# Performance work log

Measured on AMD Instinct MI355X. Metric: run time of the kernel, lower is better.

## Reference

```python
import jax, jax.numpy as jnp
import numpy as np
import math

HID = 1152
NH = 16
HD = HID // NH            # 72
P = 2
DEPTH = 4
MLP_M = int(2.0 / 3.0 * int(HID * 4.0))  # 3072 (SwiGLU inner)
FREQ = 256
NCLS = 1000
ROPE_THETA = 10000.0


def rms_norm(x, w, eps=1e-6):
    return x * jax.lax.rsqrt(jnp.mean(jnp.square(x), axis=-1, keepdims=True) + eps) * w


def rotate_half(x):
    # interleaved pairs (a, b) -> (-b, a)
    x2 = x.reshape(x.shape[:-1] + (x.shape[-1] // 2, 2))
    a, b = x2[..., 0], x2[..., 1]
    return jnp.stack((-b, a), axis=-1).reshape(x.shape)


def make_rope(S, head_dim, theta=ROPE_THETA):
    # VisionRotaryEmbedder: per-axis rope dim = head_dim//2, 2 spatial axes concat
    d = head_dim // 2
    f = 1.0 / theta ** (jnp.arange(0, d, 2)[: d // 2].astype(jnp.float32) / d)
    fr = jnp.arange(S, dtype=jnp.float32)[:, None] * f[None, :]   # [S, d//2]
    fr = jnp.repeat(fr, 2, axis=-1)                               # [S, d]
    grid = jnp.concatenate(
        [jnp.broadcast_to(fr[:, None, :], (S, S, d)),
         jnp.broadcast_to(fr[None, :, :], (S, S, d))], axis=-1)   # [S, S, head_dim]
    grid = grid.reshape(S * S, head_dim)
    return jnp.cos(grid), jnp.sin(grid)


def timestep_embedding(t, dim=FREQ, max_period=10000.0):
    half = dim // 2
    freqs = jnp.exp(-math.log(max_period) * jnp.arange(half, dtype=jnp.float32) / half)
    args = t[:, None].astype(jnp.float32) * freqs[None, :]
    return jnp.concatenate([jnp.cos(args), jnp.sin(args)], axis=-1)


def setup_inputs() -> dict:
    key = jax.random.key(0)
    ks = jax.random.split(key, 24)
    s = 0.02
    B, C, H, W = 2, 4, 64, 64
    d = {
        'x': jax.random.normal(ks[0], (B, C, H, W), jnp.float32),
        't': jax.random.uniform(ks[1], (B,), jnp.float32),
        'y': jax.random.randint(ks[2], (B,), 0, NCLS),
        'patch_w': jax.random.normal(ks[3], (P * P * C, HID), jnp.float32) * s,
        'patch_b': jnp.zeros((HID,), jnp.float32),
        't_w1': jax.random.normal(ks[4], (FREQ, HID), jnp.float32) * s,
        't_b1': jnp.zeros((HID,), jnp.float32),
        't_w2': jax.random.normal(ks[5], (HID, HID), jnp.float32) * s,
        't_b2': jnp.zeros((HID,), jnp.float32),
        'y_table': jax.random.normal(ks[6], (NCLS + 1, HID), jnp.float32) * s,
        'norm1_w': jnp.ones((DEPTH, HID), jnp.float32),
        'qkv_w': jax.random.normal(ks[7], (DEPTH, HID, 3 * HID), jnp.float32) * s,
        'qkv_b': jnp.zeros((DEPTH, 3 * HID), jnp.float32),
        'out_w': jax.random.normal(ks[8], (DEPTH, HID, HID), jnp.float32) * s,
        'out_b': jnp.zeros((DEPTH, HID), jnp.float32),
        'norm2_w': jnp.ones((DEPTH, HID), jnp.float32),
        'mlp_w12': jax.random.normal(ks[9], (DEPTH, HID, 2 * MLP_M), jnp.float32) * s,
        'mlp_b12': jnp.zeros((DEPTH, 2 * MLP_M), jnp.float32),
        'mlp_w3': jax.random.normal(ks[10], (DEPTH, MLP_M, HID), jnp.float32) * s,
        'mlp_b3': jnp.zeros((DEPTH, HID), jnp.float32),
        'adaln_w': jax.random.normal(ks[11], (DEPTH, HID, 4 * HID), jnp.float32) * s,
        'adaln_b': jnp.zeros((DEPTH, 4 * HID), jnp.float32),
        'fnorm_w': jnp.ones((HID,), jnp.float32),
        'fadaln_w': jax.random.normal(ks[12], (HID, 2 * HID), jnp.float32) * s,
        'fadaln_b': jnp.zeros((2 * HID,), jnp.float32),
        'flin_w': jax.random.normal(ks[13], (HID, P * P * C), jnp.float32) * s,
        'flin_b': jnp.zeros((P * P * C,), jnp.float32),
    }
    return d


def reference(x, t, y, patch_w, patch_b, t_w1, t_b1, t_w2, t_b2, y_table,
              norm1_w, qkv_w, qkv_b, out_w, out_b, norm2_w,
              mlp_w12, mlp_b12, mlp_w3, mlp_b3, adaln_w, adaln_b,
              fnorm_w, fadaln_w, fadaln_b, flin_w, flin_b):
    B, C, H, W = x.shape
    S = H // P
    L = S * S
    # patchify -> [B, L, P*P*C] -> linear embed
    tok = x.reshape(B, C, S, P, S, P).transpose(0, 2, 4, 3, 5, 1).reshape(B, L, P * P * C)
    h = tok @ patch_w + patch_b
    # conditioning: timestep MLP + class embedding
    temb = timestep_embedding(t)
    temb = jax.nn.silu(temb @ t_w1 + t_b1) @ t_w2 + t_b2
    c = temb + y_table[y]
    c_silu = jax.nn.silu(c)
    cos, sin = make_rope(S, HD)  # [L, HD]
    scale = 1.0 / math.sqrt(HD)

    def block(hx, p):
        n1w, qw, qb, ow, ob, n2w, w12, b12, w3, b3, aw, ab = p
        mod = c_silu @ aw + ab  # [B, 4*HID]
        s_msa, g_msa, s_mlp, g_mlp = jnp.split(mod, 4, axis=-1)
        hmod = rms_norm(hx, n1w) * (1.0 + s_msa[:, None, :])
        qkv = (hmod @ qw + qb).reshape(B, L, 3, NH, HD)
        qkv = jnp.swapaxes(qkv, 1, 3)  # [B, NH, 3, L, HD]
        q, k, v = qkv[:, :, 0], qkv[:, :, 1], qkv[:, :, 2]
        q = q * cos + rotate_half(q) * sin
        k = k * cos + rotate_half(k) * sin
        w = jax.nn.softmax(jnp.einsum('bhqd,bhkd->bhqk', q, k) * scale, axis=-1)
        o = jnp.einsum('bhqk,bhkd->bhqd', w, v)
        o = jnp.swapaxes(o, 1, 2).reshape(B, L, HID) @ ow + ob
        hx = hx + g_msa[:, None, :] * o
        hmod2 = rms_norm(hx, n2w) * (1.0 + s_mlp[:, None, :])
        x12 = hmod2 @ w12 + b12
        x1, x2 = jnp.split(x12, 2, axis=-1)
        m = (jax.nn.silu(x1) * x2) @ w3 + b3
        hx = hx + g_mlp[:, None, :] * m
        return hx, None

    h, _ = jax.lax.scan(block, h, (norm1_w, qkv_w, qkv_b, out_w, out_b, norm2_w,
                                   mlp_w12, mlp_b12, mlp_w3, mlp_b3, adaln_w, adaln_b))

    # final layer: shift+scale modulation then zero-init linear (random here)
    fmod = c_silu @ fadaln_w + fadaln_b
    shift, fscale = jnp.split(fmod, 2, axis=-1)
    hf = rms_norm(h, fnorm_w) * (1.0 + fscale[:, None, :]) + shift[:, None, :]
    out = hf @ flin_w + flin_b  # [B, L, P*P*C]
    out = out.reshape(B, S, S, P, P, C).transpose(0, 5, 1, 3, 2, 4).reshape(B, C, H, W)
    return out
```

## Files before the change

### kernel.cpp

```cpp
#include <hip/hip_runtime.h>
#include <hip/hip_bf16.h>

#define HIDN 1152
#define NHEAD 16
#define HDIM 72
#define LTOK 1024
#define MTOK 2048
#define MLPM 3072

typedef short bf16x8 __attribute__((ext_vector_type(8)));
typedef float f32x4 __attribute__((ext_vector_type(4)));

__device__ __forceinline__ void gload16(const void* g, void* l) {
    __builtin_amdgcn_global_load_lds(
        (const __attribute__((address_space(1))) void*)g,
        (__attribute__((address_space(3))) void*)l,
        16, 0, 0);
}

__global__ __launch_bounds__(256) void k_patch(const float* __restrict__ x,
        const float* __restrict__ pw, const float* __restrict__ pb,
        float* __restrict__ h) {
    int m = blockIdx.x;
    int b = m >> 10, l = m & 1023;
    int si = l >> 5, sj = l & 31;
    __shared__ float toks[16];
    int tid = threadIdx.x;
    if (tid < 16) {
        int pi = tid >> 3, pj = (tid >> 2) & 1, c = tid & 3;
        toks[tid] = x[((size_t)(b*4 + c)*64 + si*2 + pi)*64 + sj*2 + pj];
    }
    __syncthreads();
    for (int o = tid; o < HIDN; o += 256) {
        float acc = pb[o];
        #pragma unroll
        for (int kk = 0; kk < 16; ++kk) acc += toks[kk] * pw[kk*HIDN + o];
        h[(size_t)m*HIDN + o] = acc;
    }
}

__global__ __launch_bounds__(256) void k_temb1_v2(const float* __restrict__ t,
        const float* __restrict__ w1, const float* __restrict__ b1,
        float* __restrict__ temb1) {
    int jt = blockIdx.x, b = blockIdx.y;
    int tid = threadIdx.x;
    __shared__ float emb[256];
    __shared__ float red[128];
    float tv = t[b];
    if (tid < 128) { float f = __expf(-logf(10000.f) * (float)tid / 128.f);        emb[tid] = cosf(tv * f); }
    else           { float f = __expf(-logf(10000.f) * (float)(tid - 128) / 128.f); emb[tid] = sinf(tv * f); }
    __syncthreads();
    int o = jt*128 + (tid & 127), s = tid >> 7;
    float acc = 0.f;
    for (int k = s*128; k < s*128 + 128; ++k) acc += emb[k] * w1[(size_t)k*HIDN + o];
    if (s) red[tid & 127] = acc;
    __syncthreads();
    if (!s) {
        float v = acc + red[tid] + b1[o];
        temb1[b*HIDN + o] = v / (1.f + __expf(-v));
    }
}

__global__ __launch_bounds__(256) void k_csilu_s1(const float* __restrict__ temb1,
        const float* __restrict__ w2, float* __restrict__ csilup) {
    int jt = blockIdx.x, kz = blockIdx.y;
    int tid = threadIdx.x;
    __shared__ float t1s[2][288];
    __shared__ float red[2][128];
    for (int i = tid; i < 576; i += 256)
        t1s[i/288][i%288] = temb1[(i/288)*HIDN + kz*288 + (i%288)];
    __syncthreads();
    int o = jt*128 + (tid & 127), s = tid >> 7;
    float a0 = 0.f, a1 = 0.f;
    for (int i = s*144; i < s*144 + 144; ++i) {
        float wv = w2[(size_t)(kz*288 + i)*HIDN + o];
        a0 += t1s[0][i]*wv; a1 += t1s[1][i]*wv;
    }
    if (s) { red[0][tid & 127] = a0; red[1][tid & 127] = a1; }
    __syncthreads();
    if (!s) {
        csilup[(kz*2 + 0)*HIDN + o] = a0 + red[0][tid];
        csilup[(kz*2 + 1)*HIDN + o] = a1 + red[1][tid];
    }
}

__global__ __launch_bounds__(128) void k_csilu_s2(const float* __restrict__ csilup,
        const float* __restrict__ b2, const float* __restrict__ ytab,
        const int* __restrict__ y, float* __restrict__ csilu) {
    int o = blockIdx.x*128 + threadIdx.x;
    int b = blockIdx.y;
    float acc = b2[o] + ytab[(size_t)y[b]*HIDN + o];
    #pragma unroll
    for (int kz = 0; kz < 4; ++kz) acc += csilup[(kz*2 + b)*HIDN + o];
    csilu[b*HIDN + o] = acc / (1.f + __expf(-acc));
}

__global__ __launch_bounds__(256) void k_cond_s1(const float* __restrict__ csilu,
        const float* __restrict__ adaln_w, const float* __restrict__ fadaln_w,
        float* __restrict__ condp) {
    int ct = blockIdx.x, kz = blockIdx.y;
    int tid = threadIdx.x;
    int c0 = ct*128;
    const float* Wb; int rstride;
    if (c0 < 18432) { int d = c0/4608; Wb = adaln_w + (size_t)d*HIDN*4608 + (c0 % 4608); rstride = 4608; }
    else            { Wb = fadaln_w + (c0 - 18432); rstride = 2304; }
    __shared__ float cs[2][288];
    __shared__ float red[2][128];
    for (int i = tid; i < 576; i += 256)
        cs[i/288][i%288] = csilu[(i/288)*HIDN + kz*288 + (i%288)];
    __syncthreads();
    int o = tid & 127, s = tid >> 7;
    float a0 = 0.f, a1 = 0.f;
    for (int i = s*144; i < s*144 + 144; ++i) {
        float wv = Wb[(size_t)(kz*288 + i)*rstride + o];
        a0 += cs[0][i]*wv; a1 += cs[1][i]*wv;
    }
    if (s) { red[0][o] = a0; red[1][o] = a1; }
    __syncthreads();
    if (!s) {
        condp[((size_t)kz*2 + 0)*20736 + c0 + o] = a0 + red[0][o];
        condp[((size_t)kz*2 + 1)*20736 + c0 + o] = a1 + red[1][o];
    }
}

__global__ __launch_bounds__(256) void k_cond_s2(const float* __restrict__ condp,
        const float* __restrict__ adaln_b, const float* __restrict__ fadaln_b,
        float* __restrict__ modb, float* __restrict__ fmod) {
    int c = blockIdx.x*256 + threadIdx.x;
    int b = blockIdx.y;
    float acc = 0.f;
    #pragma unroll
    for (int kz = 0; kz < 4; ++kz) acc += condp[((size_t)kz*2 + b)*20736 + c];
    if (c < 18432) {
        int d = c/4608, j = c%4608;
        modb[((size_t)d*2 + b)*4608 + j] = acc + adaln_b[(size_t)d*4608 + j];
    } else {
        int j = c - 18432;
        fmod[(size_t)b*2304 + j] = acc + fadaln_b[j];
    }
}

__global__ __launch_bounds__(256) void k_rope(float* __restrict__ cosb, float* __restrict__ sinb) {
    int idx = blockIdx.x*256 + threadIdx.x;
    if (idx >= LTOK*HDIM) return;
    int l = idx / HDIM, dd = idx % HDIM;
    int i = l >> 5, j = l & 31;
    int pos = (dd < 36) ? i : j;
    int mm = ((dd < 36) ? dd : dd - 36) >> 1;
    float f = __expf(-logf(10000.f) * (float)mm / 18.f);
    float fr = (float)pos * f;
    cosb[idx] = cosf(fr);
    sinb[idx] = sinf(fr);
}

__global__ __launch_bounds__(256) void k_rms(const float* __restrict__ hx,
        const float* __restrict__ nw, const float* __restrict__ smod,
        __hip_bfloat16* __restrict__ outp) {
    int m = blockIdx.x; int b = m >> 10;
    int tid = threadIdx.x;
    const float* row = hx + (size_t)m*HIDN;
    float part = 0.f;
    for (int j = tid; j < HIDN; j += 256) { float v = row[j]; part += v*v; }
    for (int off = 32; off; off >>= 1) part += __shfl_xor(part, off);
    __shared__ float wsum[4];
    if ((tid & 63) == 0) wsum[tid >> 6] = part;
    __syncthreads();
    float rs = rsqrtf((wsum[0]+wsum[1]+wsum[2]+wsum[3]) * (1.f/HIDN) + 1e-6f);
    const float* sb = smod + (size_t)b*4608;
    __hip_bfloat16* orow = outp + (size_t)m*HIDN;
    for (int j = tid; j < HIDN; j += 256)
        orow[j] = __float2bfloat16(row[j] * rs * nw[j] * (1.f + sb[j]));
}

__global__ __launch_bounds__(256) void k_castT(const float* __restrict__ W,
        __hip_bfloat16* __restrict__ Wt, int K, int N) {
    __shared__ float tile[32][33];
    int n0 = blockIdx.x*32, k0 = blockIdx.y*32;
    int tx = threadIdx.x, ty = threadIdx.y;
    for (int i = ty; i < 32; i += 8)
        tile[i][tx] = W[(size_t)(k0+i)*N + n0 + tx];
    __syncthreads();
    for (int i = ty; i < 32; i += 8)
        Wt[(size_t)(n0+i)*K + k0 + tx] = __float2bfloat16(tile[tx][i]);
}

template<int EPI, typename OutT>
__global__ __launch_bounds__(256) void k_gemm_bf16(
        const __hip_bfloat16* __restrict__ A,
        const __hip_bfloat16* __restrict__ Wt,
        const float* __restrict__ bias,
        OutT* __restrict__ C, int M, int N, int K,
        const float* __restrict__ gate) {
    __shared__ __hip_bfloat16 Asm[128*64];
    __shared__ __hip_bfloat16 Bsm[128*64];
    int tid = threadIdx.x;
    int lane = tid & 63, w = tid >> 6;
    int wr = w >> 1, wc = w & 1;
    int m0 = blockIdx.y * 128, n0 = blockIdx.x * 128;
    f32x4 acc[4][4] = {};
    int lr = lane >> 3, ls = lane & 7;
    int swz = ls ^ (lr & 7);
    int x7 = lane & 7;
    const __hip_bfloat16* Ag = A  + (size_t)(m0 + lr)*K + swz*8;
    const __hip_bfloat16* Bg = Wt + (size_t)(n0 + lr)*K + swz*8;
    for (int k0 = 0; k0 < K; k0 += 64) {
        #pragma unroll
        for (int i = 0; i < 4; ++i) {
            int seg = w*4 + i;
            gload16(Ag + (size_t)(seg*8)*K + k0, (char*)Asm + seg*1024);
            gload16(Bg + (size_t)(seg*8)*K + k0, (char*)Bsm + seg*1024);
        }
        __syncthreads();
        #pragma unroll
        for (int kk = 0; kk < 2; ++kk) {
            bf16x8 af[4], bfr[4];
            #pragma unroll
            for (int m = 0; m < 4; ++m) {
                int row = wr*64 + m*16 + (lane&15);
                af[m] = *(const bf16x8*)(Asm + row*64 + (((kk*4 + (lane>>4)) ^ x7) * 8));
            }
            #pragma unroll
            for (int n = 0; n < 4; ++n) {
                int col = wc*64 + n*16 + (lane&15);
                bfr[n] = *(const bf16x8*)(Bsm + col*64 + (((kk*4 + (lane>>4)) ^ x7) * 8));
            }
            #pragma unroll
            for (int m = 0; m < 4; ++m)
                #pragma unroll
                for (int n = 0; n < 4; ++n)
                    acc[m][n] = __builtin_amdgcn_mfma_f32_16x16x32_bf16(af[m], bfr[n], acc[m][n], 0, 0, 0);
        }
        __syncthreads();
    }
    int r0 = (lane >> 4) * 4;
    int ccol = lane & 15;
    #pragma unroll
    for (int m = 0; m < 4; ++m) {
        #pragma unroll
        for (int rr = 0; rr < 4; ++rr) {
            int row = m0 + wr*64 + m*16 + r0 + rr;
            int bi = row >> 10;
            #pragma unroll
            for (int n = 0; n < 4; ++n) {
                int col = n0 + wc*64 + n*16 + ccol;
                float val = acc[m][n][rr] + bias[col];
                if (EPI == 0) {
                    C[(size_t)row*N + col] = (OutT)__float2bfloat16(val);
                } else {
                    ((float*)C)[(size_t)row*N + col] += gate[(size_t)bi*4608 + col] * val;
                }
            }
        }
    }
}

__global__ __launch_bounds__(256) void k_gemm64(
        const __hip_bfloat16* __restrict__ A,
        const __hip_bfloat16* __restrict__ Wt,
        const float* __restrict__ bias,
        float* __restrict__ C, int M, int N, int K,
        const float* __restrict__ gate) {
    __shared__ __hip_bfloat16 Asm[64*64];
    __shared__ __hip_bfloat16 Bsm[128*64];
    int tid = threadIdx.x;
    int lane = tid & 63, w = tid >> 6;
    int wr = w >> 1, wc = w & 1;
    int m0 = blockIdx.y * 64, n0 = blockIdx.x * 128;
    f32x4 acc[2][4] = {};
    int lr = lane >> 3, ls = lane & 7;
    int swz = ls ^ (lr & 7);
    int x7 = lane & 7;
    const __hip_bfloat16* Ag = A  + (size_t)(m0 + lr)*K + swz*8;
    const __hip_bfloat16* Bg = Wt + (size_t)(n0 + lr)*K + swz*8;
    for (int k0 = 0; k0 < K; k0 += 64) {
        #pragma unroll
        for (int i = 0; i < 2; ++i) {
            int seg = w*2 + i;
            gload16(Ag + (size_t)(seg*8)*K + k0, (char*)Asm + seg*1024);
        }
        #pragma unroll
        for (int i = 0; i < 4; ++i) {
            int seg = w*4 + i;
            gload16(Bg + (size_t)(seg*8)*K + k0, (char*)Bsm + seg*1024);
        }
        __syncthreads();
        #pragma unroll
        for (int kk = 0; kk < 2; ++kk) {
            bf16x8 af[2], bfr[4];
            #pragma unroll
            for (int m = 0; m < 2; ++m) {
                int row = wr*32 + m*16 + (lane&15);
                af[m] = *(const bf16x8*)(Asm + row*64 + (((kk*4 + (lane>>4)) ^ x7) * 8));
            }
            #pragma unroll
            for (int n = 0; n < 4; ++n) {
                int col = wc*64 + n*16 + (lane&15);
                bfr[n] = *(const bf16x8*)(Bsm + col*64 + (((kk*4 + (lane>>4)) ^ x7) * 8));
            }
            #pragma unroll
            for (int m = 0; m < 2; ++m)
                #pragma unroll
                for (int n = 0; n < 4; ++n)
                    acc[m][n] = __builtin_amdgcn_mfma_f32_16x16x32_bf16(af[m], bfr[n], acc[m][n], 0, 0, 0);
        }
        __syncthreads();
    }
    int r0 = (lane >> 4) * 4;
    int ccol = lane & 15;
    #pragma unroll
    for (int m = 0; m < 2; ++m) {
        #pragma unroll
        for (int rr = 0; rr < 4; ++rr) {
            int row = m0 + wr*32 + m*16 + r0 + rr;
            int bi = row >> 10;
            #pragma unroll
            for (int n = 0; n < 4; ++n) {
                int col = n0 + wc*64 + n*16 + ccol;
                float val = acc[m][n][rr] + bias[col];
                C[(size_t)row*N + col] += gate[(size_t)bi*4608 + col] * val;
            }
        }
    }
}

__global__ __launch_bounds__(256) void k_ropesplit(const __hip_bfloat16* __restrict__ qkv,
        const float* __restrict__ cosb, const float* __restrict__ sinb,
        __hip_bfloat16* __restrict__ q, __hip_bfloat16* __restrict__ k,
        __hip_bfloat16* __restrict__ v) {
    int idx = blockIdx.x*256 + threadIdx.x;
    if (idx >= 2*NHEAD*LTOK*36) return;
    int dp = idx % 36;
    int l  = (idx / 36) % LTOK;
    int h  = (idx / (36*LTOK)) % NHEAD;
    int b  = idx / (36*LTOK*NHEAD);
    int d0 = dp*2;
    size_t src = (size_t)(b*LTOK + l)*3456 + h*HDIM + d0;
    float qe = __bfloat162float(qkv[src]),        qo = __bfloat162float(qkv[src+1]);
    float ke = __bfloat162float(qkv[src+HIDN]),   ko = __bfloat162float(qkv[src+HIDN+1]);
    float ce = cosb[l*HDIM+d0], co = cosb[l*HDIM+d0+1];
    float se = sinb[l*HDIM+d0], so = sinb[l*HDIM+d0+1];
    size_t dst = (size_t)((b*NHEAD + h)*LTOK + l)*HDIM + d0;
    q[dst]   = __float2bfloat16(qe*ce - qo*se);
    q[dst+1] = __float2bfloat16(qo*co + qe*so);
    k[dst]   = __float2bfloat16(ke*ce - ko*se);
    k[dst+1] = __float2bfloat16(ko*co + ke*so);
    size_t vdst = ((size_t)(b*NHEAD + h)*HDIM + d0)*LTOK + l;
    v[vdst]        = qkv[src+2*HIDN];
    v[vdst+LTOK]   = qkv[src+2*HIDN+1];
}

__global__ __launch_bounds__(256) void k_attn_mfma(
        const __hip_bfloat16* __restrict__ q,
        const __hip_bfloat16* __restrict__ k,
        const __hip_bfloat16* __restrict__ vt,
        __hip_bfloat16* __restrict__ o) {
    int blk = blockIdx.x;
    int qt = blk & 15, h = (blk >> 4) & 15, b = blk >> 8;
    const float scale = 0.117851130f;
    __shared__ __hip_bfloat16 Ksm[2][64*72];
    __shared__ __hip_bfloat16 Vsm[2][72*64];
    __shared__ __hip_bfloat16 Psm[4][16*72];
    int tid = threadIdx.x, lane = tid & 63, w = tid >> 6;
    int l15 = lane & 15, g = lane >> 4;
    const __hip_bfloat16* qg = q  + ((size_t)(b*NHEAD + h)*LTOK + qt*64)*HDIM;
    const __hip_bfloat16* kg = k  + (size_t)(b*NHEAD + h)*LTOK*HDIM;
    const __hip_bfloat16* vg = vt + (size_t)(b*NHEAD + h)*HDIM*LTOK;
    const bf16x8 z = {};

    bf16x8 qf[3];
    {
        const __hip_bfloat16* qrow = qg + (w*16 + l15)*HDIM;
        qf[0] = *(const bf16x8*)(qrow + g*8);
        qf[1] = *(const bf16x8*)(qrow + 32 + g*8);
        qf[2] = (g == 0) ? *(const bf16x8*)(qrow + 64) : z;
    }
    int vsw  = ((lane & 7) ^ (lane >> 3)) * 8;
    int vrow = lane >> 3;

    f32x4 oacc[5] = {};
    float mold[4] = {-1e30f, -1e30f, -1e30f, -1e30f};
    float lsum[4] = {};

    {
        const __hip_bfloat16* ktg = kg;
        const __hip_bfloat16* vtg = vg;
        for (int s = w; s < 9; s += 4) {
            gload16(ktg + s*512 + lane*8, (char*)&Ksm[0][0] + s*1024);
            gload16(vtg + (size_t)(s*8 + vrow)*LTOK + vsw, (char*)&Vsm[0][0] + s*1024);
        }
    }
    __syncthreads();

    for (int kt2 = 0; kt2 < 16; ++kt2) {
        int cur = kt2 & 1;
        if (kt2 < 15) {
            const __hip_bfloat16* ktg = kg + (size_t)(kt2+1)*64*HDIM;
            const __hip_bfloat16* vtg = vg + (kt2+1)*64;
            for (int s = w; s < 9; s += 4) {
                gload16(ktg + s*512 + lane*8, (char*)&Ksm[cur^1][0] + s*1024);
                gload16(vtg + (size_t)(s*8 + vrow)*LTOK + vsw, (char*)&Vsm[cur^1][0] + s*1024);
            }
        }
        const __hip_bfloat16* Kc = Ksm[cur];
        const __hip_bfloat16* Vc = Vsm[cur];
        f32x4 st[4] = {};
        __builtin_amdgcn_s_setprio(1);
        #pragma unroll
        for (int t = 0; t < 4; ++t) {
            const __hip_bfloat16* krow = Kc + (t*16 + l15)*72;
            bf16x8 kf0 = *(const bf16x8*)(krow + g*8);
            bf16x8 kf1 = *(const bf16x8*)(krow + 32 + g*8);
            bf16x8 kf2 = (g == 0) ? *(const bf16x8*)(krow + 64) : z;
            st[t] = __builtin_amdgcn_mfma_f32_16x16x32_bf16(qf[0], kf0, st[t], 0, 0, 0);
            st[t] = __builtin_amdgcn_mfma_f32_16x16x32_bf16(qf[1], kf1, st[t], 0, 0, 0);
            st[t] = __builtin_amdgcn_mfma_f32_16x16x32_bf16(qf[2], kf2, st[t], 0, 0, 0);
        }
        __builtin_amdgcn_s_setprio(0);
        #pragma unroll
        for (int r = 0; r < 4; ++r) {
            float mt = fmaxf(fmaxf(st[0][r], st[1][r]), fmaxf(st[2][r], st[3][r]));
            mt = fmaxf(mt, __shfl_xor(mt, 1));
            mt = fmaxf(mt, __shfl_xor(mt, 2));
            mt = fmaxf(mt, __shfl_xor(mt, 4));
            mt = fmaxf(mt, __shfl_xor(mt, 8));
            float mn = fmaxf(mold[r], mt);
            float corr = __expf((mold[r] - mn) * scale);
            mold[r] = mn;
            lsum[r] *= corr;
            #pragma unroll
            for (int dt = 0; dt < 5; ++dt) oacc[dt][r] *= corr;
            float rs = 0.f;
            #pragma unroll
            for (int t = 0; t < 4; ++t) {
                float p = __expf((st[t][r] - mn) * scale);
                rs += p;
                Psm[w][(g*4 + r)*72 + t*16 + l15] = __float2bfloat16(p);
            }
            rs += __shfl_xor(rs, 1);
            rs += __shfl_xor(rs, 2);
            rs += __shfl_xor(rs, 4);
            rs += __shfl_xor(rs, 8);
            lsum[r] += rs;
        }
        bf16x8 pa0 = *(const bf16x8*)(&Psm[w][l15*72 + g*8]);
        bf16x8 pa1 = *(const bf16x8*)(&Psm[w][l15*72 + 32 + g*8]);
        int cswz = (l15 & 7)*8;
        __builtin_amdgcn_s_setprio(1);
        #pragma unroll
        for (int dt = 0; dt < 5; ++dt) {
            int row = dt*16 + l15;
            bool valid = (dt < 4) | (l15 < 8);
            bf16x8 vf0 = valid ? *(const bf16x8*)(Vc + row*64 + ((g*8) ^ cswz)) : z;
            bf16x8 vf1 = valid ? *(const bf16x8*)(Vc + row*64 + ((32 + g*8) ^ cswz)) : z;
            oacc[dt] = __builtin_amdgcn_mfma_f32_16x16x32_bf16(pa0, vf0, oacc[dt], 0, 0, 0);
            oacc[dt] = __builtin_amdgcn_mfma_f32_16x16x32_bf16(pa1, vf1, oacc[dt], 0, 0, 0);
        }
        __builtin_amdgcn_s_setprio(0);
        __syncthreads();
    }
    #pragma unroll
    for (int r = 0; r < 4; ++r) {
        float inv = 1.f / lsum[r];
        int row = qt*64 + w*16 + g*4 + r;
        __hip_bfloat16* op = o + ((size_t)b*LTOK + row)*HIDN + h*HDIM;
        #pragma unroll
        for (int dt = 0; dt < 5; ++dt) {
            int d = dt*16 + l15;
            if (d < HDIM) op[d] = __float2bfloat16(oacc[dt][r] * inv);
        }
    }
}

__global__ __launch_bounds__(256) void k_glu(const __hip_bfloat16* __restrict__ x12,
        __hip_bfloat16* __restrict__ mh) {
    int idx = blockIdx.x*256 + threadIdx.x;
    int m = idx / 384, jj = (idx % 384)*8;
    bf16x8 v1 = *(const bf16x8*)(x12 + (size_t)m*6144 + jj);
    bf16x8 v2 = *(const bf16x8*)(x12 + (size_t)m*6144 + MLPM + jj);
    bf16x8 ov;
    #pragma unroll
    for (int i = 0; i < 8; ++i) {
        short s1 = v1[i], s2 = v2[i];
        float x1 = __bfloat162float(*(__hip_bfloat16*)&s1);
        float x2 = __bfloat162float(*(__hip_bfloat16*)&s2);
        __hip_bfloat16 r = __float2bfloat16(x1 / (1.f + __expf(-x1)) * x2);
        ov[i] = *(short*)&r;
    }
    *(bf16x8*)(mh + (size_t)m*MLPM + jj) = ov;
}

__global__ __launch_bounds__(256) void k_final(const float* __restrict__ hx,
        const float* __restrict__ fnw, const float* __restrict__ fmod,
        const float* __restrict__ flw, const float* __restrict__ flb,
        float* __restrict__ out) {
    int m = blockIdx.x; int b = m >> 10, l = m & 1023;
    int tid = threadIdx.x;
    const float* row = hx + (size_t)m*HIDN;
    float part = 0.f;
    for (int j = tid; j < HIDN; j += 256) { float v2 = row[j]; part += v2*v2; }
    for (int off = 32; off; off >>= 1) part += __shfl_xor(part, off);
    __shared__ float wsum[4];
    __shared__ float hfs[HIDN];
    __shared__ float red[4][16];
    if ((tid & 63) == 0) wsum[tid >> 6] = part;
    __syncthreads();
    float rs = rsqrtf((wsum[0]+wsum[1]+wsum[2]+wsum[3]) * (1.f/HIDN) + 1e-6f);
    const float* fm = fmod + (size_t)b*2304;
    for (int j = tid; j < HIDN; j += 256)
        hfs[j] = row[j] * rs * fnw[j] * (1.f + fm[HIDN + j]) + fm[j];
    __syncthreads();
    float pacc[16] = {};
    for (int j = tid; j < HIDN; j += 256) {
        float hv = hfs[j];
        #pragma unroll
        for (int kk = 0; kk < 16; ++kk) pacc[kk] += hv * flw[j*16 + kk];
    }
    #pragma unroll
    for (int kk = 0; kk < 16; ++kk)
        for (int off = 32; off; off >>= 1) pacc[kk] += __shfl_xor(pacc[kk], off);
    if ((tid & 63) == 0) {
        int w = tid >> 6;
        #pragma unroll
        for (int kk = 0; kk < 16; ++kk) red[w][kk] = pacc[kk];
    }
    __syncthreads();
    if (tid < 16) {
        float val = red[0][tid] + red[1][tid] + red[2][tid] + red[3][tid] + flb[tid];
        int pi = tid >> 3, pj = (tid >> 2) & 1, c = tid & 3;
        int si = l >> 5, sj = l & 31;
        out[((size_t)(b*4 + c)*64 + si*2 + pi)*64 + sj*2 + pj] = val;
    }
}

extern "C" void kernel_launch(void* const* d_in, const int* in_sizes, int n_in,
                              void* d_out, int out_size, void* d_ws, size_t ws_size,
                              hipStream_t stream) {
    const float* x        = (const float*)d_in[0];
    const float* t        = (const float*)d_in[1];
    const int*   y        = (const int*)  d_in[2];
    const float* patch_w  = (const float*)d_in[3];
    const float* patch_b  = (const float*)d_in[4];
    const float* t_w1     = (const float*)d_in[5];
    const float* t_b1     = (const float*)d_in[6];
    const float* t_w2     = (const float*)d_in[7];
    const float* t_b2     = (const float*)d_in[8];
    const float* y_table  = (const float*)d_in[9];
    const float* norm1_w  = (const float*)d_in[10];
    const float* qkv_w    = (const float*)d_in[11];
    const float* qkv_b    = (const float*)d_in[12];
    const float* out_w    = (const float*)d_in[13];
    const float* out_b    = (const float*)d_in[14];
    const float* norm2_w  = (const float*)d_in[15];
    const float* mlp_w12  = (const float*)d_in[16];
    const float* mlp_b12  = (const float*)d_in[17];
    const float* mlp_w3   = (const float*)d_in[18];
    const float* mlp_b3   = (const float*)d_in[19];
    const float* adaln_w  = (const float*)d_in[20];
    const float* adaln_b  = (const float*)d_in[21];
    const float* fnorm_w  = (const float*)d_in[22];
    const float* fadaln_w = (const float*)d_in[23];
    const float* fadaln_b = (const float*)d_in[24];
    const float* flin_w   = (const float*)d_in[25];
    const float* flin_b   = (const float*)d_in[26];

    char* base = (char*)d_ws;
    float*          hx    = (float*)(base);
    __hip_bfloat16* qkvbf = (__hip_bfloat16*)(base +  9437184);
    __hip_bfloat16* qbf   = (__hip_bfloat16*)(base + 34603008);
    __hip_bfloat16* kbf   = (__hip_bfloat16*)(base + 39321600);
    __hip_bfloat16* vbf   = (__hip_bfloat16*)(base + 44040192);
    __hip_bfloat16* hbf   = (__hip_bfloat16*)(base + 48758784);
    __hip_bfloat16* mhbf  = qbf;
    __hip_bfloat16* wtb   = (__hip_bfloat16*)(base + 53477376);
    float* temb1 = (float*)(base + 85327872);
    float* csilu = (float*)(base + 85337088);
    float* modb  = (float*)(base + 85346304);
    float* fmod  = (float*)(base + 85493760);
    float* cosb  = (float*)(base + 85512192);
    float* sinb  = (float*)(base + 85807104);
    float* condp = (float*)(base + 86102016);
    float* csilup= (float*)(base + 86765568);

    __hip_bfloat16* wt_qkv = wtb;
    __hip_bfloat16* wt_out = wt_qkv + 3456*1152;
    __hip_bfloat16* wt_m12 = wt_out + 1152*1152;
    __hip_bfloat16* wt_m3  = wt_m12 + 6144*1152;

    k_patch<<<2048, 256, 0, stream>>>(x, patch_w, patch_b, hx);
    k_temb1_v2<<<dim3(9,2), 256, 0, stream>>>(t, t_w1, t_b1, temb1);
    k_csilu_s1<<<dim3(9,4), 256, 0, stream>>>(temb1, t_w2, csilup);
    k_csilu_s2<<<dim3(9,2), 128, 0, stream>>>(csilup, t_b2, y_table, y, csilu);
    k_cond_s1<<<dim3(162,4), 256, 0, stream>>>(csilu, adaln_w, fadaln_w, condp);
    k_cond_s2<<<dim3(81,2), 256, 0, stream>>>(condp, adaln_b, fadaln_b, modb, fmod);
    k_rope<<<288, 256, 0, stream>>>(cosb, sinb);

    for (int d = 0; d < 4; ++d) {
        const float* modd = modb + (size_t)d*2*4608;
        k_castT<<<dim3(108,36), dim3(32,8), 0, stream>>>(qkv_w  + (size_t)d*HIDN*3456, wt_qkv, HIDN, 3456);
        k_castT<<<dim3( 36,36), dim3(32,8), 0, stream>>>(out_w  + (size_t)d*HIDN*HIDN, wt_out, HIDN, HIDN);
        k_castT<<<dim3(192,36), dim3(32,8), 0, stream>>>(mlp_w12+ (size_t)d*HIDN*6144, wt_m12, HIDN, 6144);
        k_castT<<<dim3( 36,96), dim3(32,8), 0, stream>>>(mlp_w3 + (size_t)d*MLPM*HIDN, wt_m3,  MLPM, HIDN);

        k_rms<<<2048, 256, 0, stream>>>(hx, norm1_w + d*HIDN, modd + 0*HIDN, hbf);
        k_gemm_bf16<0, __hip_bfloat16><<<dim3(27,16), 256, 0, stream>>>(hbf, wt_qkv,
                qkv_b + d*3456, qkvbf, MTOK, 3456, HIDN, nullptr);
        k_ropesplit<<<4608, 256, 0, stream>>>(qkvbf, cosb, sinb, qbf, kbf, vbf);
        k_attn_mfma<<<512, 256, 0, stream>>>(qbf, kbf, vbf, hbf);
        k_gemm64<<<dim3(9,32), 256, 0, stream>>>(hbf, wt_out,
                out_b + d*HIDN, hx, MTOK, HIDN, HIDN, modd + 1*HIDN);
        k_rms<<<2048, 256, 0, stream>>>(hx, norm2_w + d*HIDN, modd + 2*HIDN, hbf);
        k_gemm_bf16<0, __hip_bfloat16><<<dim3(48,16), 256, 0, stream>>>(hbf, wt_m12,
                mlp_b12 + d*6144, qkvbf, MTOK, 6144, HIDN, nullptr);
        k_glu<<<3072, 256, 0, stream>>>(qkvbf, mhbf);
        k_gemm64<<<dim3(9,32), 256, 0, stream>>>(mhbf, wt_m3,
                mlp_b3 + d*HIDN, hx, MTOK, HIDN, MLPM, modd + 3*HIDN);
    }
    k_final<<<2048, 256, 0, stream>>>(hx, fnorm_w, fmod, flin_w, flin_b, (float*)d_out);
}
```

Measured before the change: 1.097 ms.

## Batch weight casts, fuse SwiGLU into GEMM epilogue, split-K attention with merge

Result: slower. 1.126 ms (+2.6%).

```diff
diff --git a/kernel.cpp b/kernel.cpp
--- a/kernel.cpp
+++ b/kernel.cpp
@@ -172,16 +172,29 @@
         orow[j] = __float2bfloat16(row[j] * rs * nw[j] * (1.f + sb[j]));
 }
 
-__global__ __launch_bounds__(256) void k_castT(const float* __restrict__ W,
-        __hip_bfloat16* __restrict__ Wt, int K, int N) {
+__global__ __launch_bounds__(256) void k_castT_all(
+        const float* __restrict__ qkv_w, const float* __restrict__ out_w,
+        const float* __restrict__ m12_w, const float* __restrict__ m3_w,
+        __hip_bfloat16* __restrict__ wtb) {
     __shared__ float tile[32][33];
-    int n0 = blockIdx.x*32, k0 = blockIdx.y*32;
+    int bid = blockIdx.x;
+    int layer = bid / 15552, r = bid % 15552;
+    const float* W; __hip_bfloat16* Wt; int K, N, nt, t; bool glu = false;
+    __hip_bfloat16* bl = wtb + (size_t)layer*15925248;
+    if (r < 3888)       { t = r;         nt = 108; K = 1152; N = 3456; W = qkv_w + (size_t)layer*K*N; Wt = bl; }
+    else if (r < 5184)  { t = r - 3888;  nt = 36;  K = 1152; N = 1152; W = out_w + (size_t)layer*K*N; Wt = bl + 3981312; }
+    else if (r < 12096) { t = r - 5184;  nt = 192; K = 1152; N = 6144; W = m12_w + (size_t)layer*K*N; Wt = bl + 5308416; glu = true; }
+    else                { t = r - 12096; nt = 36;  K = 3072; N = 1152; W = m3_w  + (size_t)layer*K*N; Wt = bl + 12386304; }
+    int n0 = (t % nt)*32, k0 = (t / nt)*32;
     int tx = threadIdx.x, ty = threadIdx.y;
     for (int i = ty; i < 32; i += 8)
         tile[i][tx] = W[(size_t)(k0+i)*N + n0 + tx];
     __syncthreads();
-    for (int i = ty; i < 32; i += 8)
-        Wt[(size_t)(n0+i)*K + k0 + tx] = __float2bfloat16(tile[tx][i]);
+    for (int i = ty; i < 32; i += 8) {
+        int n = n0 + i;
+        int np = glu ? ((n < 3072) ? 2*n : 2*(n - 3072) + 1) : n;
+        Wt[(size_t)np*K + k0 + tx] = __float2bfloat16(tile[tx][i]);
+    }
 }
 
 template<int EPI, typename OutT>
@@ -243,11 +256,19 @@
             #pragma unroll
             for (int n = 0; n < 4; ++n) {
                 int col = n0 + wc*64 + n*16 + ccol;
-                float val = acc[m][n][rr] + bias[col];
                 if (EPI == 0) {
+                    float val = acc[m][n][rr] + bias[col];
                     C[(size_t)row*N + col] = (OutT)__float2bfloat16(val);
+                } else if (EPI == 1) {
+                    float val = acc[m][n][rr] + bias[col];
+                    ((float*)C)[(size_t)row*N + col] += gate[(size_t)bi*4608 + col] * val;
                 } else {
-                    ((float*)C)[(size_t)row*N + col] += gate[(size_t)bi*4608 + col] * val;
+                    float val = acc[m][n][rr] + bias[(col & 1) ? 3072 + (col >> 1) : (col >> 1)];
+                    float other = __shfl_xor(val, 1);
+                    if (!(lane & 1)) {
+                        float res = val / (1.f + __expf(-val)) * other;
+                        ((__hip_bfloat16*)C)[(size_t)row*(N>>1) + (col>>1)] = __float2bfloat16(res);
+                    }
                 }
             }
         }
@@ -353,9 +374,9 @@
         const __hip_bfloat16* __restrict__ q,
         const __hip_bfloat16* __restrict__ k,
         const __hip_bfloat16* __restrict__ vt,
-        __hip_bfloat16* __restrict__ o) {
+        float* __restrict__ po, float2* __restrict__ ml) {
     int blk = blockIdx.x;
-    int qt = blk & 15, h = (blk >> 4) & 15, b = blk >> 8;
+    int split = blk & 1, qt = (blk >> 1) & 15, h = (blk >> 5) & 15, b = blk >> 9;
     const float scale = 0.117851130f;
     __shared__ __hip_bfloat16 Ksm[2][64*72];
     __shared__ __hip_bfloat16 Vsm[2][72*64];
@@ -382,8 +403,8 @@
     float lsum[4] = {};
 
     {
-        const __hip_bfloat16* ktg = kg;
-        const __hip_bfloat16* vtg = vg;
+        const __hip_bfloat16* ktg = kg + (size_t)(split*8)*64*HDIM;
+        const __hip_bfloat16* vtg = vg + split*8*64;
         for (int s = w; s < 9; s += 4) {
             gload16(ktg + s*512 + lane*8, (char*)&Ksm[0][0] + s*1024);
             gload16(vtg + (size_t)(s*8 + vrow)*LTOK + vsw, (char*)&Vsm[0][0] + s*1024);
@@ -391,11 +412,11 @@
     }
     __syncthreads();
 
-    for (int kt2 = 0; kt2 < 16; ++kt2) {
+    for (int kt2 = 0; kt2 < 8; ++kt2) {
         int cur = kt2 & 1;
-        if (kt2 < 15) {
-            const __hip_bfloat16* ktg = kg + (size_t)(kt2+1)*64*HDIM;
-            const __hip_bfloat16* vtg = vg + (kt2+1)*64;
+        if (kt2 < 7) {
+            const __hip_bfloat16* ktg = kg + (size_t)(split*8 + kt2 + 1)*64*HDIM;
+            const __hip_bfloat16* vtg = vg + (split*8 + kt2 + 1)*64;
             for (int s = w; s < 9; s += 4) {
                 gload16(ktg + s*512 + lane*8, (char*)&Ksm[cur^1][0] + s*1024);
                 gload16(vtg + (size_t)(s*8 + vrow)*LTOK + vsw, (char*)&Vsm[cur^1][0] + s*1024);
@@ -460,33 +481,35 @@
     }
     #pragma unroll
     for (int r = 0; r < 4; ++r) {
-        float inv = 1.f / lsum[r];
         int row = qt*64 + w*16 + g*4 + r;
-        __hip_bfloat16* op = o + ((size_t)b*LTOK + row)*HIDN + h*HDIM;
+        size_t rowg = (size_t)(b*NHEAD + h)*LTOK + row;
+        float* op = po + ((size_t)split*32768 + rowg)*72;
         #pragma unroll
         for (int dt = 0; dt < 5; ++dt) {
             int d = dt*16 + l15;
-            if (d < HDIM) op[d] = __float2bfloat16(oacc[dt][r] * inv);
-        }
-    }
-}
-
-__global__ __launch_bounds__(256) void k_glu(const __hip_bfloat16* __restrict__ x12,
-        __hip_bfloat16* __restrict__ mh) {
-    int idx = blockIdx.x*256 + threadIdx.x;
-    int m = idx / 384, jj = (idx % 384)*8;
-    bf16x8 v1 = *(const bf16x8*)(x12 + (size_t)m*6144 + jj);
-    bf16x8 v2 = *(const bf16x8*)(x12 + (size_t)m*6144 + MLPM + jj);
-    bf16x8 ov;
-    #pragma unroll
-    for (int i = 0; i < 8; ++i) {
-        short s1 = v1[i], s2 = v2[i];
-        float x1 = __bfloat162float(*(__hip_bfloat16*)&s1);
-        float x2 = __bfloat162float(*(__hip_bfloat16*)&s2);
-        __hip_bfloat16 r = __float2bfloat16(x1 / (1.f + __expf(-x1)) * x2);
-        ov[i] = *(short*)&r;
-    }
-    *(bf16x8*)(mh + (size_t)m*MLPM + jj) = ov;
+            if (d < HDIM) op[d] = oacc[dt][r];
+        }
+        if (l15 == 0) ml[(size_t)split*32768 + rowg] = make_float2(mold[r], lsum[r]);
+    }
+}
+
+__global__ __launch_bounds__(256) void k_attn_merge(const float* __restrict__ po,
+        const float2* __restrict__ ml, __hip_bfloat16* __restrict__ o) {
+    const float scale = 0.117851130f;
+    int bl = blockIdx.x;
+    int b = bl >> 10, l = bl & 1023;
+    int tid = threadIdx.x;
+    for (int idx = tid; idx < HIDN; idx += 256) {
+        int h = idx / HDIM, d = idx % HDIM;
+        size_t rowg = (size_t)(b*NHEAD + h)*LTOK + l;
+        float2 m0 = ml[rowg], m1 = ml[32768 + rowg];
+        float mn = fmaxf(m0.x, m1.x);
+        float e0 = __expf((m0.x - mn) * scale);
+        float e1 = __expf((m1.x - mn) * scale);
+        float denom = e0*m0.y + e1*m1.y;
+        float v = (e0*po[rowg*72 + d] + e1*po[(32768 + rowg)*72 + d]) / denom;
+        o[((size_t)b*LTOK + l)*HIDN + idx] = __float2bfloat16(v);
+    }
 }
 
 __global__ __launch_bounds__(256) void k_final(const float* __restrict__ hx,
@@ -572,19 +595,16 @@
     __hip_bfloat16* hbf   = (__hip_bfloat16*)(base + 48758784);
     __hip_bfloat16* mhbf  = qbf;
     __hip_bfloat16* wtb   = (__hip_bfloat16*)(base + 53477376);
-    float* temb1 = (float*)(base + 85327872);
-    float* csilu = (float*)(base + 85337088);
-    float* modb  = (float*)(base + 85346304);
-    float* fmod  = (float*)(base + 85493760);
-    float* cosb  = (float*)(base + 85512192);
-    float* sinb  = (float*)(base + 85807104);
-    float* condp = (float*)(base + 86102016);
-    float* csilup= (float*)(base + 86765568);
-
-    __hip_bfloat16* wt_qkv = wtb;
-    __hip_bfloat16* wt_out = wt_qkv + 3456*1152;
-    __hip_bfloat16* wt_m12 = wt_out + 1152*1152;
-    __hip_bfloat16* wt_m3  = wt_m12 + 6144*1152;
+    float*  po   = (float*)(base + 180879360);
+    float2* mlbuf= (float2*)(base + 199753728);
+    float* temb1 = (float*)(base + 200278016);
+    float* csilu = (float*)(base + 200287232);
+    float* modb  = (float*)(base + 200296448);
+    float* fmod  = (float*)(base + 200443904);
+    float* cosb  = (float*)(base + 200462336);
+    float* sinb  = (float*)(base + 200757248);
+    float* condp = (float*)(base + 201052160);
+    float* csilup= (float*)(base + 201715712);
 
     k_patch<<<2048, 256, 0, stream>>>(x, patch_w, patch_b, hx);
     k_temb1_v2<<<dim3(9,2), 256, 0, stream>>>(t, t_w1, t_b1, temb1);
@@ -593,25 +613,27 @@
     k_cond_s1<<<dim3(162,4), 256, 0, stream>>>(csilu, adaln_w, fadaln_w, condp);
     k_cond_s2<<<dim3(81,2), 256, 0, stream>>>(condp, adaln_b, fadaln_b, modb, fmod);
     k_rope<<<288, 256, 0, stream>>>(cosb, sinb);
+    k_castT_all<<<62208, dim3(32,8), 0, stream>>>(qkv_w, out_w, mlp_w12, mlp_w3, wtb);
 
     for (int d = 0; d < 4; ++d) {
         const float* modd = modb + (size_t)d*2*4608;
-        k_castT<<<dim3(108,36), dim3(32,8), 0, stream>>>(qkv_w  + (size_t)d*HIDN*3456, wt_qkv, HIDN, 3456);
-        k_castT<<<dim3( 36,36), dim3(32,8), 0, stream>>>(out_w  + (size_t)d*HIDN*HIDN, wt_out, HIDN, HIDN);
-        k_castT<<<dim3(192,36), dim3(32,8), 0, stream>>>(mlp_w12+ (size_t)d*HIDN*6144, wt_m12, HIDN, 6144);
-        k_castT<<<dim3( 36,96), dim3(32,8), 0, stream>>>(mlp_w3 + (size_t)d*MLPM*HIDN, wt_m3,  MLPM, HIDN);
+        __hip_bfloat16* wl = wtb + (size_t)d*15925248;
+        __hip_bfloat16* wt_qkv = wl;
+        __hip_bfloat16* wt_out = wl + 3981312;
+        __hip_bfloat16* wt_m12 = wl + 5308416;
+        __hip_bfloat16* wt_m3  = wl + 12386304;
 
         k_rms<<<2048, 256, 0, stream>>>(hx, norm1_w + d*HIDN, modd + 0*HIDN, hbf);
         k_gemm_bf16<0, __hip_bfloat16><<<dim3(27,16), 256, 0, stream>>>(hbf, wt_qkv,
                 qkv_b + d*3456, qkvbf, MTOK, 3456, HIDN, nullptr);
         k_ropesplit<<<4608, 256, 0, stream>>>(qkvbf, cosb, sinb, qbf, kbf, vbf);
-        k_attn_mfma<<<512, 256, 0, stream>>>(qbf, kbf, vbf, hbf);
+        k_attn_mfma<<<1024, 256, 0, stream>>>(qbf, kbf, vbf, po, mlbuf);
+        k_attn_merge<<<2048, 256, 0, stream>>>(po, mlbuf, hbf);
         k_gemm64<<<dim3(9,32), 256, 0, stream>>>(hbf, wt_out,
                 out_b + d*HIDN, hx, MTOK, HIDN, HIDN, modd + 1*HIDN);
         k_rms<<<2048, 256, 0, stream>>>(hx, norm2_w + d*HIDN, modd + 2*HIDN, hbf);
-        k_gemm_bf16<0, __hip_bfloat16><<<dim3(48,16), 256, 0, stream>>>(hbf, wt_m12,
-                mlp_b12 + d*6144, qkvbf, MTOK, 6144, HIDN, nullptr);
-        k_glu<<<3072, 256, 0, stream>>>(qkvbf, mhbf);
+        k_gemm_bf16<2, __hip_bfloat16><<<dim3(48,16), 256, 0, stream>>>(hbf, wt_m12,
+                mlp_b12 + d*6144, mhbf, MTOK, 6144, HIDN, nullptr);
         k_gemm64<<<dim3(9,32), 256, 0, stream>>>(mhbf, wt_m3,
                 mlp_b3 + d*HIDN, hx, MTOK, HIDN, MLPM, modd + 3*HIDN);
     }
```
